# Optimization experiments

Measured on AMD Instinct MI355X. Metric: run time of the kernel, lower is better.

Reference implementation:

```python
import jax, jax.numpy as jnp
import numpy as np

NUM_OPS = 100_000
NUM_MACH = 512
H = 128
OPF = 6
MF = 2
L = 2
N_PREC = 800_000
N_CHALF = 800_000  # compat edges per direction
EPS = 1e-5


def setup_inputs() -> dict:
    key = jax.random.key(0)
    ks = jax.random.split(key, 20)
    op_features = jax.random.normal(ks[0], (NUM_OPS, OPF), dtype=jnp.float32)
    machine_features = jax.random.normal(ks[1], (NUM_MACH, MF), dtype=jnp.float32)
    prec_src = jax.random.randint(ks[2], (N_PREC,), 0, NUM_OPS, dtype=jnp.int32)
    prec_tgt = jax.random.randint(ks[3], (N_PREC,), 0, NUM_OPS, dtype=jnp.int32)
    precedence_edges = jnp.stack([prec_src, prec_tgt])  # [2, N_PREC]
    op_idx = jax.random.randint(ks[4], (N_CHALF,), 0, NUM_OPS, dtype=jnp.int32)
    m_idx = jax.random.randint(ks[5], (N_CHALF,), 0, NUM_MACH, dtype=jnp.int32)
    # bidirectional pairs in unified node space (machines offset by NUM_OPS)
    src = jnp.concatenate([op_idx, m_idx + NUM_OPS])
    tgt = jnp.concatenate([m_idx + NUM_OPS, op_idx])
    compatibility_edges = jnp.stack([src, tgt])  # [2, 2*N_CHALF]
    s = 0.05
    op_emb_W = jax.random.normal(ks[6], (H, OPF), dtype=jnp.float32) * s
    op_emb_b = jnp.zeros((H,), jnp.float32)
    mach_emb_W = jax.random.normal(ks[7], (H, MF), dtype=jnp.float32) * s
    mach_emb_b = jnp.zeros((H,), jnp.float32)
    prec_W = jax.random.normal(ks[8], (L, H, H), dtype=jnp.float32) * s
    prec_b = jax.random.normal(ks[9], (L, H), dtype=jnp.float32) * s
    compat_W = jax.random.normal(ks[10], (L, H, H), dtype=jnp.float32) * s
    compat_b = jax.random.normal(ks[11], (L, H), dtype=jnp.float32) * s
    op_ln_g = jnp.ones((L, H), jnp.float32)
    op_ln_b = jnp.zeros((L, H), jnp.float32)
    mach_ln_g = jnp.ones((L, H), jnp.float32)
    mach_ln_b = jnp.zeros((L, H), jnp.float32)
    return dict(op_features=op_features, machine_features=machine_features,
                precedence_edges=precedence_edges, compatibility_edges=compatibility_edges,
                op_emb_W=op_emb_W, op_emb_b=op_emb_b, mach_emb_W=mach_emb_W, mach_emb_b=mach_emb_b,
                prec_W=prec_W, prec_b=prec_b, compat_W=compat_W, compat_b=compat_b,
                op_ln_g=op_ln_g, op_ln_b=op_ln_b, mach_ln_g=mach_ln_g, mach_ln_b=mach_ln_b)


def _layer_norm(x, g, b):
    mu = jnp.mean(x, axis=-1, keepdims=True)
    var = jnp.mean(jnp.square(x - mu), axis=-1, keepdims=True)
    return (x - mu) * jax.lax.rsqrt(var + EPS) * g + b


def _scatter_mean(vals, idx, mask, n):
    # vals [E,H], idx [E], mask [E] bool (or None); mean over incoming edges, count clamped >= 1
    if mask is not None:
        vals = jnp.where(mask[:, None], vals, 0.0)
        idx = jnp.where(mask, idx, 0)
        ones = mask.astype(vals.dtype)
    else:
        ones = jnp.ones(idx.shape, vals.dtype)
    sums = jax.ops.segment_sum(vals, idx, num_segments=n)
    cnts = jax.ops.segment_sum(ones, idx, num_segments=n)
    return sums / jnp.maximum(cnts, 1.0)[:, None]


def _forward(op_features, machine_features, precedence_edges, compatibility_edges,
             op_emb_W, op_emb_b, mach_emb_W, mach_emb_b,
             prec_W, prec_b, compat_W, compat_b,
             op_ln_g, op_ln_b, mach_ln_g, mach_ln_b):
    num_ops = op_features.shape[0]
    num_mach = machine_features.shape[0]
    op_emb = op_features @ op_emb_W.T + op_emb_b
    mach_emb = machine_features @ mach_emb_W.T + mach_emb_b

    p_src, p_tgt = precedence_edges[0], precedence_edges[1]
    c_src, c_tgt = compatibility_edges[0], compatibility_edges[1]
    op2m = (c_src < num_ops) & (c_tgt >= num_ops)
    m2o = (c_src >= num_ops) & (c_tgt < num_ops)
    o2m_src = jnp.where(op2m, c_src, 0)
    o2m_tgt = jnp.where(op2m, c_tgt - num_ops, 0)
    m2o_src = jnp.where(m2o, c_src - num_ops, 0)
    m2o_tgt = jnp.where(m2o, c_tgt, 0)

    for l in range(L):
        # precedence (op -> op): linear-then-gather == gather-then-linear
        op_t = op_emb @ prec_W[l].T + prec_b[l]            # [num_ops, H]
        op_emb_prec = _scatter_mean(op_t[p_src], p_tgt, None, num_ops)
        # compatibility, shared linear for both directions
        op_c = op_emb @ compat_W[l].T + compat_b[l]        # [num_ops, H]
        mach_c = mach_emb @ compat_W[l].T + compat_b[l]    # [num_mach, H]
        mach_emb_compat = _scatter_mean(op_c[o2m_src], o2m_tgt, op2m, num_mach)
        op_emb_compat = _scatter_mean(mach_c[m2o_src], m2o_tgt, m2o, num_ops)
        op_emb = _layer_norm(op_emb + op_emb_prec + op_emb_compat, op_ln_g[l], op_ln_b[l])
        mach_emb = _layer_norm(mach_emb + mach_emb_compat, mach_ln_g[l], mach_ln_b[l])
    return op_emb, mach_emb


def reference(op_features, machine_features, precedence_edges, compatibility_edges,
              op_emb_W, op_emb_b, mach_emb_W, mach_emb_b,
              prec_W, prec_b, compat_W, compat_b,
              op_ln_g, op_ln_b, mach_ln_g, mach_ln_b):
    return _forward(op_features, machine_features, precedence_edges, compatibility_edges,
                    op_emb_W, op_emb_b, mach_emb_W, mach_emb_b,
                    prec_W, prec_b, compat_W, compat_b,
                    op_ln_g, op_ln_b, mach_ln_g, mach_ln_b)
```

## Files before the change

kernel.cpp:

```cpp
#include <hip/hip_runtime.h>
#include <hip/hip_bf16.h>

#define NUM_OPS   100000
#define NUM_MACH  512
#define HDIM      128
#define P1        100352
#define NHIST     200704
#define NBLK      196
#define NCOARSE   784
#define NBC       256
#define NBM       256
#define MHWORDS   (NUM_MACH * NBM)
#define NBLK_M    128
#define NBLK_T    (NBLK + NBLK_M)

typedef short short8 __attribute__((ext_vector_type(8)));
typedef float floatx4 __attribute__((ext_vector_type(4)));

__device__ __forceinline__ unsigned short f2bf(float f) {
    unsigned u = __float_as_uint(f);
    unsigned r = (u + 0x7FFFu + ((u >> 16) & 1u)) >> 16;
    return (unsigned short)r;
}
__device__ __forceinline__ float bf2f(unsigned short u) {
    return __uint_as_float(((unsigned)u) << 16);
}

__global__ void k_prep(const float* __restrict__ Fo, const float* __restrict__ Fm,
                       const float* __restrict__ Wo, const float* __restrict__ bo,
                       const float* __restrict__ Wm, const float* __restrict__ bm,
                       const float* __restrict__ Wp, const float* __restrict__ Wc,
                       float* __restrict__ op_emb, unsigned short* __restrict__ op_ebf,
                       float* __restrict__ mach_emb, unsigned short* __restrict__ Wb) {
    int idx = blockIdx.x * blockDim.x + threadIdx.x;
    if (idx < NUM_OPS * HDIM) {
        int r = idx >> 7, h = idx & 127;
        const float* f = Fo + (size_t)r * 6;
        const float* w = Wo + (size_t)h * 6;
        float s = bo[h];
#pragma unroll
        for (int i = 0; i < 6; ++i) s += f[i] * w[i];
        op_emb[idx] = s;
        op_ebf[idx] = f2bf(s);
        return;
    }
    idx -= NUM_OPS * HDIM;
    if (idx < NUM_MACH * HDIM) {
        int r = idx >> 7, h = idx & 127;
        const float* f = Fm + (size_t)r * 2;
        const float* w = Wm + (size_t)h * 2;
        mach_emb[idx] = bm[h] + f[0] * w[0] + f[1] * w[1];
        return;
    }
    idx -= NUM_MACH * HDIM;
    if (idx < 2 * 128 * 256) {
        int l = idx >> 15, h = (idx >> 8) & 127, k = idx & 255;
        float v = (k < 128) ? Wp[(size_t)l * 16384 + h * 128 + k]
                            : Wc[(size_t)l * 16384 + h * 128 + (k - 128)];
        Wb[idx] = f2bf(v);
    }
}

__global__ __launch_bounds__(256) void k_front(const int* __restrict__ prec_e, int nprec,
                                               const int* __restrict__ comp_e, int E, int M,
                                               int* __restrict__ chist_bh,
                                               int* __restrict__ mach_bh) {
    __shared__ int hc[NCOARSE];
    __shared__ int hm[NUM_MACH];
    for (int i = threadIdx.x; i < NCOARSE; i += 256) hc[i] = 0;
    for (int i = threadIdx.x; i < NUM_MACH; i += 256) hm[i] = 0;
    __syncthreads();
    int NT = nprec + E;
    int ch = (NT + NBC - 1) / NBC;
    int i0 = blockIdx.x * ch, i1 = min(NT, i0 + ch);
    for (int i = i0 + threadIdx.x; i < i1; i += 256) {
        int key;
        if (i < nprec) key = prec_e[nprec + i];
        else {
            int e = i - nprec;
            key = P1 + comp_e[e];
            atomicAdd(&hm[comp_e[E + e] - M], 1);
        }
        atomicAdd(&hc[key >> 8], 1);
    }
    __syncthreads();
    for (int i = threadIdx.x; i < NCOARSE; i += 256)
        chist_bh[i * NBC + blockIdx.x] = hc[i];
    for (int i = threadIdx.x; i < NUM_MACH; i += 256)
        mach_bh[i * NBC + blockIdx.x] = hm[i];
}

__global__ __launch_bounds__(256) void k_cfill(const int* __restrict__ prec_e, int nprec,
                                               const int* __restrict__ comp_e, int E, int M,
                                               const int* __restrict__ scan,
                                               int* __restrict__ pairs) {
    __shared__ int cur[NCOARSE];
    for (int i = threadIdx.x; i < NCOARSE; i += 256) cur[i] = scan[i * NBC + blockIdx.x];
    __syncthreads();
    int NT = nprec + E;
    int ch = (NT + NBC - 1) / NBC;
    int i0 = blockIdx.x * ch, i1 = min(NT, i0 + ch);
    for (int i = i0 + threadIdx.x; i < i1; i += 256) {
        int key, val;
        if (i < nprec) { key = prec_e[nprec + i]; val = prec_e[i]; }
        else { int e = i - nprec; key = P1 + comp_e[e]; val = comp_e[E + e] - M; }
        int pos = atomicAdd(&cur[key >> 8], 1);
        pairs[pos] = (val << 8) | (key & 255);
    }
}

__global__ __launch_bounds__(256) void k_blocksum(const int* __restrict__ arr, int* __restrict__ partial) {
    __shared__ int sh[256];
    int b = blockIdx.x, t = threadIdx.x;
    int4 v = *(const int4*)(arr + b * 1024 + t * 4);
    sh[t] = v.x + v.y + v.z + v.w;
    __syncthreads();
    for (int o = 128; o; o >>= 1) { if (t < o) sh[t] += sh[t + o]; __syncthreads(); }
    if (!t) partial[b] = sh[0];
}

__global__ __launch_bounds__(256) void k_scanpart(const int* __restrict__ partial,
                                                  int* __restrict__ block_off) {
    __shared__ int sh[256];
    int t = threadIdx.x;
    int seg0 = blockIdx.x ? NBLK : 0;
    int n    = blockIdx.x ? NBLK_M : NBLK;
    int v = (t < n) ? partial[seg0 + t] : 0;
    sh[t] = v; __syncthreads();
    for (int o = 1; o < 256; o <<= 1) {
        int x = (t >= o) ? sh[t - o] : 0; __syncthreads();
        sh[t] += x; __syncthreads();
    }
    if (t < n) block_off[seg0 + t] = sh[t] - v;
}

__global__ __launch_bounds__(256) void k_scanwrite(const int* __restrict__ arr,
                                                   const int* __restrict__ block_off,
                                                   int* __restrict__ rs) {
    __shared__ int sh[256];
    int b = blockIdx.x, t = threadIdx.x;
    int base_i = b * 1024 + t * 4;
    int4 v = *(const int4*)(arr + base_i);
    int tsum = v.x + v.y + v.z + v.w;
    sh[t] = tsum; __syncthreads();
    for (int o = 1; o < 256; o <<= 1) {
        int x = (t >= o) ? sh[t - o] : 0; __syncthreads();
        sh[t] += x; __syncthreads();
    }
    int off = block_off[b] + sh[t] - tsum;
    int4 r; r.x = off; r.y = off + v.x; r.z = off + v.x + v.y; r.w = off + v.x + v.y + v.z;
    *(int4*)(rs + base_i) = r;
}

__global__ __launch_bounds__(256) void k_finefill(const int* __restrict__ scans, int NT,
                                                  const int* __restrict__ pairs,
                                                  int* __restrict__ rs,
                                                  int* __restrict__ bucket_all,
                                                  const int* __restrict__ comp_e, int E, int M,
                                                  int* __restrict__ bucket_mach,
                                                  int* __restrict__ mach_rs) {
    int t = threadIdx.x;
    if (blockIdx.x < NCOARSE) {
        __shared__ int hh[256];
        __shared__ int ex[256];
        __shared__ int cu[256];
        int b = blockIdx.x;
        int s = scans[b * NBC];
        int e = (b == NCOARSE - 1) ? NT : scans[(b + 1) * NBC];
        hh[t] = 0;
        __syncthreads();
        for (int i = s + t; i < e; i += 256) atomicAdd(&hh[pairs[i] & 255], 1);
        __syncthreads();
        int v = hh[t];
        ex[t] = v; __syncthreads();
        for (int o = 1; o < 256; o <<= 1) {
            int x = (t >= o) ? ex[t - o] : 0; __syncthreads();
            ex[t] += x; __syncthreads();
        }
        int start = s + ex[t] - v;
        rs[b * 256 + t] = start;
        cu[t] = start;
        __syncthreads();
        for (int i = s + t; i < e; i += 256) {
            int p = pairs[i];
            int pos = atomicAdd(&cu[p & 255], 1);
            bucket_all[pos] = ((unsigned)p) >> 8;
        }
    } else {
        __shared__ int cur[NUM_MACH];
        int blk = blockIdx.x - NCOARSE;
        const int* moff = scans + NHIST;
        for (int i = t; i < NUM_MACH; i += 256) cur[i] = moff[i * NBM + blk];
        if (blk == 0) {
            for (int m = t; m < NUM_MACH; m += 256) mach_rs[m] = moff[m * NBM];
            if (t == 0) mach_rs[NUM_MACH] = E;
        }
        __syncthreads();
        int nprec = NT - E;
        int chNT = (NT + NBC - 1) / NBC;
        int e0 = blk * chNT - nprec;       if (e0 < 0) e0 = 0;
        int e1 = (blk + 1) * chNT - nprec; if (e1 > E) e1 = E;
        for (int e = e0 + t; e < e1; e += 256) {
            int m = comp_e[E + e] - M;
            int op = comp_e[e];
            int pos = atomicAdd(&cur[m], 1);
            bucket_mach[pos] = op;
        }
    }
}

__global__ __launch_bounds__(256) void k_aggmg(
    const unsigned short* __restrict__ op_ebf, const float* __restrict__ mach_emb,
    const int* __restrict__ rs, const int* __restrict__ bucket_all,
    unsigned short* __restrict__ Ab, int* __restrict__ flags, int M,
    const int* __restrict__ mach_rs, const int* __restrict__ bucket_mach,
    float* __restrict__ mach_sum, int nb_agg) {
    int wave = threadIdx.x >> 6, lane = threadIdx.x & 63;

    if ((int)blockIdx.x < nb_agg) {
        int r = blockIdx.x * 4 + wave;
        if (r >= M) return;
        int h = lane * 2;

        float a0 = 0.f, a1 = 0.f;
        int s0 = rs[r], e0 = rs[r + 1];
        for (int base = s0; base < e0; base += 64) {
            int cnt = min(64, e0 - base);
            int idx = (lane < cnt) ? bucket_all[base + lane] : 0;
            for (int j = 0; j < cnt; j += 4) {
                int i0 = __shfl(idx, j);
                int i1 = __shfl(idx, j + 1);
                int i2 = __shfl(idx, j + 2);
                int i3 = __shfl(idx, j + 3);
                ushort2 v0 = *(const ushort2*)(op_ebf + (size_t)i0 * HDIM + h);
                ushort2 v1 = *(const ushort2*)(op_ebf + (size_t)i1 * HDIM + h);
                ushort2 v2 = *(const ushort2*)(op_ebf + (size_t)i2 * HDIM + h);
                ushort2 v3 = *(const ushort2*)(op_ebf + (size_t)i3 * HDIM + h);
                a0 += bf2f(v0.x); a1 += bf2f(v0.y);
                if (j + 1 < cnt) { a0 += bf2f(v1.x); a1 += bf2f(v1.y); }
                if (j + 2 < cnt) { a0 += bf2f(v2.x); a1 += bf2f(v2.y); }
                if (j + 3 < cnt) { a0 += bf2f(v3.x); a1 += bf2f(v3.y); }
            }
        }
        float pinv = 1.f / fmaxf((float)(e0 - s0), 1.f);

        float b0 = 0.f, b1 = 0.f;
        int s1 = rs[P1 + r], e1 = rs[P1 + r + 1];
        for (int base = s1; base < e1; base += 64) {
            int cnt = min(64, e1 - base);
            int idx = (lane < cnt) ? bucket_all[base + lane] : 0;
            for (int j = 0; j < cnt; j += 4) {
                int i0 = __shfl(idx, j);
                int i1 = __shfl(idx, j + 1);
                int i2 = __shfl(idx, j + 2);
                int i3 = __shfl(idx, j + 3);
                float2 v0 = *(const float2*)(mach_emb + (size_t)i0 * HDIM + h);
                float2 v1 = *(const float2*)(mach_emb + (size_t)i1 * HDIM + h);
                float2 v2 = *(const float2*)(mach_emb + (size_t)i2 * HDIM + h);
                float2 v3 = *(const float2*)(mach_emb + (size_t)i3 * HDIM + h);
                b0 += v0.x; b1 += v0.y;
                if (j + 1 < cnt) { b0 += v1.x; b1 += v1.y; }
                if (j + 2 < cnt) { b0 += v2.x; b1 += v2.y; }
                if (j + 3 < cnt) { b0 += v3.x; b1 += v3.y; }
            }
        }
        float cinv = 1.f / fmaxf((float)(e1 - s1), 1.f);

        ushort2 pa, pb;
        pa.x = f2bf(a0 * pinv); pa.y = f2bf(a1 * pinv);
        pb.x = f2bf(b0 * cinv); pb.y = f2bf(b1 * cinv);
        *(ushort2*)(Ab + (size_t)r * 256 + h)       = pa;
        *(ushort2*)(Ab + (size_t)r * 256 + 128 + h) = pb;
        if (lane == 0) flags[r] = (e0 > s0 ? 1 : 0) | (e1 > s1 ? 2 : 0);
        return;
    }

    int b2 = blockIdx.x - nb_agg;
    int m  = b2 & 511;
    int yq = b2 >> 9;
    int g  = lane >> 4;
    int d  = (lane & 15) * 8;
    int s0 = mach_rs[m], e0 = mach_rs[m + 1];
    float a[8];
#pragma unroll
    for (int k = 0; k < 8; ++k) a[k] = 0.f;

    for (int base = s0 + (yq * 4 + wave) * 64; base < e0; base += 1024) {
        int cnt = min(64, e0 - base);
        int idx = (lane < cnt) ? bucket_mach[base + lane] : 0;
        for (int j = 0; j < cnt; j += 4) {
            int jj = j + g;
            int rowi = __shfl(idx, jj);
            short8 v = *(const short8*)(op_ebf + (size_t)rowi * HDIM + d);
            if (jj < cnt) {
#pragma unroll
                for (int k = 0; k < 8; ++k) a[k] += bf2f((unsigned short)v[k]);
            }
        }
    }
#pragma unroll
    for (int k = 0; k < 8; ++k) {
        a[k] += __shfl_xor(a[k], 16);
        a[k] += __shfl_xor(a[k], 32);
    }
    if (lane < 16) {
#pragma unroll
        for (int k = 0; k < 8; ++k)
            atomicAdd(&mach_sum[m * HDIM + d + k], a[k]);
    }
}

__global__ __launch_bounds__(256) void k_gemm_mfma(
    const unsigned short* __restrict__ Ab, const float* __restrict__ emb,
    const unsigned short* __restrict__ Wb,
    const float* __restrict__ bp, const float* __restrict__ bc,
    const int* __restrict__ flags,
    const float* __restrict__ g, const float* __restrict__ bt,
    float* __restrict__ dst, unsigned short* __restrict__ dstb, int M) {
    int wave = threadIdx.x >> 6, lane = threadIdx.x & 63;
    int m0 = blockIdx.x * 64 + wave * 16;
    if (m0 >= M) return;
    int quad = lane >> 4, col = lane & 15;

    floatx4 acc[8];
#pragma unroll
    for (int t = 0; t < 8; ++t) acc[t] = (floatx4){0.f, 0.f, 0.f, 0.f};

    const short* Arow  = (const short*)(Ab + (size_t)(m0 + col) * 256);
    const short* Wbase = (const short*)Wb;

#pragma unroll
    for (int ks = 0; ks < 8; ++ks) {
        short8 a = *(const short8*)(Arow + ks * 32 + quad * 8);
#pragma unroll
        for (int t = 0; t < 8; ++t) {
            short8 b = *(const short8*)(Wbase + (size_t)(t * 16 + col) * 256 + ks * 32 + quad * 8);
            acc[t] = __builtin_amdgcn_mfma_f32_16x16x32_bf16(a, b, acc[t], 0, 0, 0);
        }
    }

    float bpv[8], bcv[8], gv[8], btv[8];
#pragma unroll
    for (int t = 0; t < 8; ++t) {
        int c = t * 16 + col;
        bpv[t] = bp[c]; bcv[t] = bc[c]; gv[t] = g[c]; btv[t] = bt[c];
    }
#pragma unroll
    for (int reg = 0; reg < 4; ++reg) {
        int r = m0 + quad * 4 + reg;
        int fl = flags[r];
        float fp = (fl & 1) ? 1.f : 0.f, fc = (fl & 2) ? 1.f : 0.f;
        float x[8]; float s = 0.f, q = 0.f;
#pragma unroll
        for (int t = 0; t < 8; ++t) {
            float v = acc[t][reg] + emb[(size_t)r * HDIM + t * 16 + col] + fp * bpv[t] + fc * bcv[t];
            x[t] = v; s += v; q += v * v;
        }
#pragma unroll
        for (int msk = 1; msk < 16; msk <<= 1) { s += __shfl_xor(s, msk); q += __shfl_xor(q, msk); }
        float mu = s * (1.f / 128.f);
        float rstd = rsqrtf(fmaxf(q * (1.f / 128.f) - mu * mu, 0.f) + 1e-5f);
#pragma unroll
        for (int t = 0; t < 8; ++t) {
            float y = (x[t] - mu) * rstd * gv[t] + btv[t];
            dst[(size_t)r * HDIM + t * 16 + col] = y;
            if (dstb) dstb[(size_t)r * HDIM + t * 16 + col] = f2bf(y);
        }
    }
}

__global__ __launch_bounds__(128) void k_mach_update(
    const float* __restrict__ mach_emb, const float* __restrict__ mach_sum,
    const int* __restrict__ mach_rs,
    const float* __restrict__ Wc, const float* __restrict__ bc,
    const float* __restrict__ g, const float* __restrict__ bt,
    float* __restrict__ dst) {
    __shared__ float row[HDIM];
    __shared__ float red[4];
    int m = blockIdx.x, t = threadIdx.x;
    int cnt = mach_rs[m + 1] - mach_rs[m];
    float sc = (cnt > 0) ? 1.f / (float)cnt : 0.f;
    row[t] = mach_sum[m * HDIM + t] * sc;
    __syncthreads();
    float dot = bc[t];
    const float* w = Wc + (size_t)t * HDIM;
#pragma unroll 8
    for (int k = 0; k < HDIM; ++k) dot += row[k] * w[k];
    float x = mach_emb[m * HDIM + t] + ((cnt > 0) ? dot : 0.f);
    float s = x, q = x * x;
#pragma unroll
    for (int o = 32; o; o >>= 1) { s += __shfl_xor(s, o); q += __shfl_xor(q, o); }
    int wv = t >> 6;
    if ((t & 63) == 0) { red[wv * 2] = s; red[wv * 2 + 1] = q; }
    __syncthreads();
    s = red[0] + red[2]; q = red[1] + red[3];
    float mu = s * (1.f / 128.f);
    float rstd = rsqrtf(fmaxf(q * (1.f / 128.f) - mu * mu, 0.f) + 1e-5f);
    dst[m * HDIM + t] = (x - mu) * rstd * g[t] + bt[t];
}

extern "C" void kernel_launch(void* const* d_in, const int* in_sizes, int n_in,
                              void* d_out, int out_size, void* d_ws, size_t ws_size,
                              hipStream_t stream) {
    const float* op_feat    = (const float*)d_in[0];
    const float* m_feat     = (const float*)d_in[1];
    const int*   prec_e     = (const int*)d_in[2];
    const int*   comp_e     = (const int*)d_in[3];
    const float* op_emb_W   = (const float*)d_in[4];
    const float* op_emb_b   = (const float*)d_in[5];
    const float* mach_emb_W = (const float*)d_in[6];
    const float* mach_emb_b = (const float*)d_in[7];
    const float* prec_W     = (const float*)d_in[8];
    const float* prec_b     = (const float*)d_in[9];
    const float* compat_W   = (const float*)d_in[10];
    const float* compat_b   = (const float*)d_in[11];
    const float* op_ln_g    = (const float*)d_in[12];
    const float* op_ln_b    = (const float*)d_in[13];
    const float* mach_ln_g  = (const float*)d_in[14];
    const float* mach_ln_b  = (const float*)d_in[15];
    float* out = (float*)d_out;

    const int M = NUM_OPS, NM = NUM_MACH;
    const int nprec = in_sizes[2] / 2;
    const int ncomp = in_sizes[3] / 2;
    const int E = ncomp / 2;
    const int NT = nprec + E;

    float* ws = (float*)d_ws;
    size_t o = 0;
    float* op_emb   = ws + o; o += (size_t)M * HDIM;
    unsigned short* op_ebf = (unsigned short*)(ws + o); o += (size_t)M * 64;
    unsigned short* Ab = (unsigned short*)(ws + o); o += (size_t)M * 128;
    unsigned short* Wb = (unsigned short*)(ws + o); o += 32768;
    float* mach_emb = ws + o; o += (size_t)NM * HDIM;
    float* mach_sum = ws + o; o += (size_t)NM * HDIM;
    int* ip = (int*)(ws + o);
    size_t io = 0;
    int* hists     = ip + io; io += NHIST + MHWORDS;
    int* scans     = ip + io; io += NHIST + MHWORDS;
    int* rs        = ip + io; io += NHIST;
    int* mach_rs   = ip + io; io += NM + 8;
    int* partialT  = ip + io; io += 512;
    int* block_off = ip + io; io += 512;
    int* flags     = ip + io; io += M;
    int* pairs     = ip + io; io += (size_t)NT;
    int* bucket_all  = ip + io; io += (size_t)NT;
    int* bucket_mach = ip + io; io += (size_t)E;

    int* mach_bh = hists + NHIST;

    k_front<<<NBC, 256, 0, stream>>>(prec_e, nprec, comp_e, E, M, hists, mach_bh);
    k_blocksum<<<NBLK_T, 256, 0, stream>>>(hists, partialT);
    k_scanpart<<<2, 256, 0, stream>>>(partialT, block_off);
    k_scanwrite<<<NBLK_T, 256, 0, stream>>>(hists, block_off, scans);
    k_cfill<<<NBC, 256, 0, stream>>>(prec_e, nprec, comp_e, E, M, scans, pairs);
    k_finefill<<<NCOARSE + NBM, 256, 0, stream>>>(scans, NT, pairs, rs, bucket_all,
                                                  comp_e, E, M, bucket_mach, mach_rs);

    int prep_total = (M + NM) * HDIM + 2 * 128 * 256;
    k_prep<<<(prep_total + 255) / 256, 256, 0, stream>>>(
        op_feat, m_feat, op_emb_W, op_emb_b, mach_emb_W, mach_emb_b,
        prec_W, compat_W, op_emb, op_ebf, mach_emb, Wb);

    const int nb_agg = (M + 3) / 4;
    for (int l = 0; l < 2; ++l) {
        int last = (l == 1);
        const float* bpl = prec_b   + (size_t)l * HDIM;
        const float* Wc  = compat_W + (size_t)l * HDIM * HDIM;
        const float* bcl = compat_b + (size_t)l * HDIM;

        hipMemsetAsync(mach_sum, 0, (size_t)NM * HDIM * sizeof(float), stream);

        k_aggmg<<<nb_agg + NM * 4, 256, 0, stream>>>(
            op_ebf, mach_emb, rs, bucket_all, Ab, flags, M,
            mach_rs, bucket_mach, mach_sum, nb_agg);

        k_gemm_mfma<<<(M + 63) / 64, 256, 0, stream>>>(
            Ab, op_emb, Wb + (size_t)l * 128 * 256, bpl, bcl, flags,
            op_ln_g + (size_t)l * HDIM, op_ln_b + (size_t)l * HDIM,
            last ? out : op_emb, last ? nullptr : op_ebf, M);

        k_mach_update<<<NM, 128, 0, stream>>>(
            mach_emb, mach_sum, mach_rs, Wc, bcl,
            mach_ln_g + (size_t)l * HDIM, mach_ln_b + (size_t)l * HDIM,
            last ? (out + (size_t)M * HDIM) : mach_emb);
    }
}
```

Measured before the change: 579.1 us.

## Keep node embeddings in bf16 only and vectorize the per-op neighbor gathers

Drops the fp32 op embedding buffer. The GEMM/LayerNorm residual now reads the bf16 copy, and intermediate layers write only bf16, which removes a large fp32 read and write per layer. It also adds a bf16 copy of the machine embeddings. The per-op precedence and compatibility gathers switch to a shared helper that issues 16-byte loads covering four neighbor rows per wave, followed by a cross-lane reduction. The cost is rounding the residual stream to bf16, which lowers numerical accuracy.

```diff
diff --git a/kernel.cpp b/kernel.cpp
--- a/kernel.cpp
+++ b/kernel.cpp
@@ -15,6 +15,7 @@
 #define NBLK_T    (NBLK + NBLK_M)
 
 typedef short short8 __attribute__((ext_vector_type(8)));
+typedef unsigned short ushort8 __attribute__((ext_vector_type(8)));
 typedef float floatx4 __attribute__((ext_vector_type(4)));
 
 __device__ __forceinline__ unsigned short f2bf(float f) {
@@ -30,8 +31,9 @@
                        const float* __restrict__ Wo, const float* __restrict__ bo,
                        const float* __restrict__ Wm, const float* __restrict__ bm,
                        const float* __restrict__ Wp, const float* __restrict__ Wc,
-                       float* __restrict__ op_emb, unsigned short* __restrict__ op_ebf,
-                       float* __restrict__ mach_emb, unsigned short* __restrict__ Wb) {
+                       unsigned short* __restrict__ op_ebf,
+                       float* __restrict__ mach_emb, unsigned short* __restrict__ mach_ebf,
+                       unsigned short* __restrict__ Wb) {
     int idx = blockIdx.x * blockDim.x + threadIdx.x;
     if (idx < NUM_OPS * HDIM) {
         int r = idx >> 7, h = idx & 127;
@@ -40,7 +42,6 @@
         float s = bo[h];
 #pragma unroll
         for (int i = 0; i < 6; ++i) s += f[i] * w[i];
-        op_emb[idx] = s;
         op_ebf[idx] = f2bf(s);
         return;
     }
@@ -49,7 +50,9 @@
         int r = idx >> 7, h = idx & 127;
         const float* f = Fm + (size_t)r * 2;
         const float* w = Wm + (size_t)h * 2;
-        mach_emb[idx] = bm[h] + f[0] * w[0] + f[1] * w[1];
+        float s = bm[h] + f[0] * w[0] + f[1] * w[1];
+        mach_emb[idx] = s;
+        mach_ebf[idx] = f2bf(s);
         return;
     }
     idx -= NUM_MACH * HDIM;
@@ -209,68 +212,70 @@
     }
 }
 
+__device__ __forceinline__ void gather8(const unsigned short* __restrict__ src,
+                                        const int* __restrict__ bucket,
+                                        int s0, int e0, int start, int step,
+                                        int lane, int g, int d, float* a) {
+    for (int base = s0 + start; base < e0; base += step) {
+        int cnt = min(64, e0 - base);
+        int idx = (lane < cnt) ? bucket[base + lane] : 0;
+        for (int j = 0; j < cnt; j += 4) {
+            int jj = j + g;
+            int rowi = __shfl(idx, jj);
+            short8 v = *(const short8*)(src + (size_t)rowi * HDIM + d);
+            if (jj < cnt) {
+#pragma unroll
+                for (int k = 0; k < 8; ++k) a[k] += bf2f((unsigned short)v[k]);
+            }
+        }
+    }
+}
+
 __global__ __launch_bounds__(256) void k_aggmg(
-    const unsigned short* __restrict__ op_ebf, const float* __restrict__ mach_emb,
+    const unsigned short* __restrict__ op_ebf, const unsigned short* __restrict__ mach_ebf,
     const int* __restrict__ rs, const int* __restrict__ bucket_all,
     unsigned short* __restrict__ Ab, int* __restrict__ flags, int M,
     const int* __restrict__ mach_rs, const int* __restrict__ bucket_mach,
     float* __restrict__ mach_sum, int nb_agg) {
     int wave = threadIdx.x >> 6, lane = threadIdx.x & 63;
+    int g = lane >> 4;
+    int d = (lane & 15) * 8;
 
     if ((int)blockIdx.x < nb_agg) {
         int r = blockIdx.x * 4 + wave;
         if (r >= M) return;
-        int h = lane * 2;
-
-        float a0 = 0.f, a1 = 0.f;
+
+        float a[8];
+#pragma unroll
+        for (int k = 0; k < 8; ++k) a[k] = 0.f;
         int s0 = rs[r], e0 = rs[r + 1];
-        for (int base = s0; base < e0; base += 64) {
-            int cnt = min(64, e0 - base);
-            int idx = (lane < cnt) ? bucket_all[base + lane] : 0;
-            for (int j = 0; j < cnt; j += 4) {
-                int i0 = __shfl(idx, j);
-                int i1 = __shfl(idx, j + 1);
-                int i2 = __shfl(idx, j + 2);
-                int i3 = __shfl(idx, j + 3);
-                ushort2 v0 = *(const ushort2*)(op_ebf + (size_t)i0 * HDIM + h);
-                ushort2 v1 = *(const ushort2*)(op_ebf + (size_t)i1 * HDIM + h);
-                ushort2 v2 = *(const ushort2*)(op_ebf + (size_t)i2 * HDIM + h);
-                ushort2 v3 = *(const ushort2*)(op_ebf + (size_t)i3 * HDIM + h);
-                a0 += bf2f(v0.x); a1 += bf2f(v0.y);
-                if (j + 1 < cnt) { a0 += bf2f(v1.x); a1 += bf2f(v1.y); }
-                if (j + 2 < cnt) { a0 += bf2f(v2.x); a1 += bf2f(v2.y); }
-                if (j + 3 < cnt) { a0 += bf2f(v3.x); a1 += bf2f(v3.y); }
-            }
+        gather8(op_ebf, bucket_all, s0, e0, 0, 64, lane, g, d, a);
+#pragma unroll
+        for (int k = 0; k < 8; ++k) {
+            a[k] += __shfl_xor(a[k], 16);
+            a[k] += __shfl_xor(a[k], 32);
         }
         float pinv = 1.f / fmaxf((float)(e0 - s0), 1.f);
 
-        float b0 = 0.f, b1 = 0.f;
+        float b[8];
+#pragma unroll
+        for (int k = 0; k < 8; ++k) b[k] = 0.f;
         int s1 = rs[P1 + r], e1 = rs[P1 + r + 1];
-        for (int base = s1; base < e1; base += 64) {
-            int cnt = min(64, e1 - base);
-            int idx = (lane < cnt) ? bucket_all[base + lane] : 0;
-            for (int j = 0; j < cnt; j += 4) {
-                int i0 = __shfl(idx, j);
-                int i1 = __shfl(idx, j + 1);
-                int i2 = __shfl(idx, j + 2);
-                int i3 = __shfl(idx, j + 3);
-                float2 v0 = *(const float2*)(mach_emb + (size_t)i0 * HDIM + h);
-                float2 v1 = *(const float2*)(mach_emb + (size_t)i1 * HDIM + h);
-                float2 v2 = *(const float2*)(mach_emb + (size_t)i2 * HDIM + h);
-                float2 v3 = *(const float2*)(mach_emb + (size_t)i3 * HDIM + h);
-                b0 += v0.x; b1 += v0.y;
-                if (j + 1 < cnt) { b0 += v1.x; b1 += v1.y; }
-                if (j + 2 < cnt) { b0 += v2.x; b1 += v2.y; }
-                if (j + 3 < cnt) { b0 += v3.x; b1 += v3.y; }
-            }
+        gather8(mach_ebf, bucket_all, s1, e1, 0, 64, lane, g, d, b);
+#pragma unroll
+        for (int k = 0; k < 8; ++k) {
+            b[k] += __shfl_xor(b[k], 16);
+            b[k] += __shfl_xor(b[k], 32);
         }
         float cinv = 1.f / fmaxf((float)(e1 - s1), 1.f);
 
-        ushort2 pa, pb;
-        pa.x = f2bf(a0 * pinv); pa.y = f2bf(a1 * pinv);
-        pb.x = f2bf(b0 * cinv); pb.y = f2bf(b1 * cinv);
-        *(ushort2*)(Ab + (size_t)r * 256 + h)       = pa;
-        *(ushort2*)(Ab + (size_t)r * 256 + 128 + h) = pb;
+        if (lane < 16) {
+            ushort8 pa, pb;
+#pragma unroll
+            for (int k = 0; k < 8; ++k) { pa[k] = f2bf(a[k] * pinv); pb[k] = f2bf(b[k] * cinv); }
+            *(ushort8*)(Ab + (size_t)r * 256 + d)       = pa;
+            *(ushort8*)(Ab + (size_t)r * 256 + 128 + d) = pb;
+        }
         if (lane == 0) flags[r] = (e0 > s0 ? 1 : 0) | (e1 > s1 ? 2 : 0);
         return;
     }
@@ -278,26 +283,11 @@
     int b2 = blockIdx.x - nb_agg;
     int m  = b2 & 511;
     int yq = b2 >> 9;
-    int g  = lane >> 4;
-    int d  = (lane & 15) * 8;
     int s0 = mach_rs[m], e0 = mach_rs[m + 1];
     float a[8];
 #pragma unroll
     for (int k = 0; k < 8; ++k) a[k] = 0.f;
-
-    for (int base = s0 + (yq * 4 + wave) * 64; base < e0; base += 1024) {
-        int cnt = min(64, e0 - base);
-        int idx = (lane < cnt) ? bucket_mach[base + lane] : 0;
-        for (int j = 0; j < cnt; j += 4) {
-            int jj = j + g;
-            int rowi = __shfl(idx, jj);
-            short8 v = *(const short8*)(op_ebf + (size_t)rowi * HDIM + d);
-            if (jj < cnt) {
-#pragma unroll
-                for (int k = 0; k < 8; ++k) a[k] += bf2f((unsigned short)v[k]);
-            }
-        }
-    }
+    gather8(op_ebf, bucket_mach, s0, e0, (yq * 4 + wave) * 64, 1024, lane, g, d, a);
 #pragma unroll
     for (int k = 0; k < 8; ++k) {
         a[k] += __shfl_xor(a[k], 16);
@@ -311,12 +301,12 @@
 }
 
 __global__ __launch_bounds__(256) void k_gemm_mfma(
-    const unsigned short* __restrict__ Ab, const float* __restrict__ emb,
+    const unsigned short* __restrict__ Ab, const unsigned short* __restrict__ embb,
     const unsigned short* __restrict__ Wb,
     const float* __restrict__ bp, const float* __restrict__ bc,
     const int* __restrict__ flags,
     const float* __restrict__ g, const float* __restrict__ bt,
-    float* __restrict__ dst, unsigned short* __restrict__ dstb, int M) {
+    float* __restrict__ dstf, unsigned short* __restrict__ dstb, int M) {
     int wave = threadIdx.x >> 6, lane = threadIdx.x & 63;
     int m0 = blockIdx.x * 64 + wave * 16;
     if (m0 >= M) return;
@@ -353,7 +343,7 @@
         float x[8]; float s = 0.f, q = 0.f;
 #pragma unroll
         for (int t = 0; t < 8; ++t) {
-            float v = acc[t][reg] + emb[(size_t)r * HDIM + t * 16 + col] + fp * bpv[t] + fc * bcv[t];
+            float v = acc[t][reg] + bf2f(embb[(size_t)r * HDIM + t * 16 + col]) + fp * bpv[t] + fc * bcv[t];
             x[t] = v; s += v; q += v * v;
         }
 #pragma unroll
@@ -363,7 +353,7 @@
 #pragma unroll
         for (int t = 0; t < 8; ++t) {
             float y = (x[t] - mu) * rstd * gv[t] + btv[t];
-            dst[(size_t)r * HDIM + t * 16 + col] = y;
+            if (dstf) dstf[(size_t)r * HDIM + t * 16 + col] = y;
             if (dstb) dstb[(size_t)r * HDIM + t * 16 + col] = f2bf(y);
         }
     }
@@ -374,7 +364,7 @@
     const int* __restrict__ mach_rs,
     const float* __restrict__ Wc, const float* __restrict__ bc,
     const float* __restrict__ g, const float* __restrict__ bt,
-    float* __restrict__ dst) {
+    float* __restrict__ dst, unsigned short* __restrict__ dstb) {
     __shared__ float row[HDIM];
     __shared__ float red[4];
     int m = blockIdx.x, t = threadIdx.x;
@@ -396,7 +386,9 @@
     s = red[0] + red[2]; q = red[1] + red[3];
     float mu = s * (1.f / 128.f);
     float rstd = rsqrtf(fmaxf(q * (1.f / 128.f) - mu * mu, 0.f) + 1e-5f);
-    dst[m * HDIM + t] = (x - mu) * rstd * g[t] + bt[t];
+    float y = (x - mu) * rstd * g[t] + bt[t];
+    dst[m * HDIM + t] = y;
+    if (dstb) dstb[m * HDIM + t] = f2bf(y);
 }
 
 extern "C" void kernel_launch(void* const* d_in, const int* in_sizes, int n_in,
@@ -428,11 +420,11 @@
 
     float* ws = (float*)d_ws;
     size_t o = 0;
-    float* op_emb   = ws + o; o += (size_t)M * HDIM;
     unsigned short* op_ebf = (unsigned short*)(ws + o); o += (size_t)M * 64;
     unsigned short* Ab = (unsigned short*)(ws + o); o += (size_t)M * 128;
     unsigned short* Wb = (unsigned short*)(ws + o); o += 32768;
     float* mach_emb = ws + o; o += (size_t)NM * HDIM;
+    unsigned short* mach_ebf = (unsigned short*)(ws + o); o += (size_t)NM * 64;
     float* mach_sum = ws + o; o += (size_t)NM * HDIM;
     int* ip = (int*)(ws + o);
     size_t io = 0;
@@ -460,7 +452,7 @@
     int prep_total = (M + NM) * HDIM + 2 * 128 * 256;
     k_prep<<<(prep_total + 255) / 256, 256, 0, stream>>>(
         op_feat, m_feat, op_emb_W, op_emb_b, mach_emb_W, mach_emb_b,
-        prec_W, compat_W, op_emb, op_ebf, mach_emb, Wb);
+        prec_W, compat_W, op_ebf, mach_emb, mach_ebf, Wb);
 
     const int nb_agg = (M + 3) / 4;
     for (int l = 0; l < 2; ++l) {
@@ -472,17 +464,17 @@
         hipMemsetAsync(mach_sum, 0, (size_t)NM * HDIM * sizeof(float), stream);
 
         k_aggmg<<<nb_agg + NM * 4, 256, 0, stream>>>(
-            op_ebf, mach_emb, rs, bucket_all, Ab, flags, M,
+            op_ebf, mach_ebf, rs, bucket_all, Ab, flags, M,
             mach_rs, bucket_mach, mach_sum, nb_agg);
 
         k_gemm_mfma<<<(M + 63) / 64, 256, 0, stream>>>(
-            Ab, op_emb, Wb + (size_t)l * 128 * 256, bpl, bcl, flags,
+            Ab, op_ebf, Wb + (size_t)l * 128 * 256, bpl, bcl, flags,
             op_ln_g + (size_t)l * HDIM, op_ln_b + (size_t)l * HDIM,
-            last ? out : op_emb, last ? nullptr : op_ebf, M);
+            last ? out : nullptr, last ? nullptr : op_ebf, M);
 
         k_mach_update<<<NM, 128, 0, stream>>>(
             mach_emb, mach_sum, mach_rs, Wc, bcl,
             mach_ln_g + (size_t)l * HDIM, mach_ln_b + (size_t)l * HDIM,
-            last ? (out + (size_t)M * HDIM) : mach_emb);
-    }
-}
+            last ? (out + (size_t)M * HDIM) : mach_emb, last ? nullptr : mach_ebf);
+    }
+}
```

Measured after the change: 567.0 us. 1.02x faster.
